# Kernel optimization log

Measured on AMD Instinct MI355X. Metric: run time of the kernel, lower is better.

The kernel has to match this reference:

```python
import jax, jax.numpy as jnp
import numpy as np

SIGMA = 2.5
B, L, V, C = 8, 2048, 8192, 64
F = 2 * (C + 1)  # top_net in_features = 130


def rbf_interp(points_1, feats_1, points_2, sigma):
    """RBF interpolation of feats_1 at points_1 onto points_2 (atom2D torch_rbf, concat=True).
    points_1: [V,3], feats_1: [V,C], points_2: [L,3] -> [L, C+1]
    """
    # exact cdist via gram trick, [L, V]
    d2 = (jnp.sum(points_2 * points_2, -1)[:, None]
          - 2.0 * (points_2 @ points_1.T)
          + jnp.sum(points_1 * points_1, -1)[None, :])
    d = jnp.sqrt(jnp.maximum(d2, 0.0))
    w = jnp.exp(-d / sigma)                       # [L, V]
    dens = jnp.sum(w, axis=1, keepdims=True)      # [L, 1]
    w = w / dens
    # original computes weights under torch.no_grad()
    w = jax.lax.stop_gradient(w)
    dens = jax.lax.stop_gradient(dens)
    feats_2 = w @ feats_1                         # [L, C]
    return jnp.concatenate([feats_2, dens], axis=1)


def setup_inputs() -> dict:
    key = jax.random.key(0)
    ks = jax.random.split(key, 8)
    return {
        "locs_left": jax.random.normal(ks[0], (B, L, 3), jnp.float32),
        "locs_right": jax.random.normal(ks[1], (B, L, 3), jnp.float32),
        "verts_left": jax.random.normal(ks[2], (B, V, 3), jnp.float32),
        "verts_right": jax.random.normal(ks[3], (B, V, 3), jnp.float32),
        "feats_left": jax.random.normal(ks[4], (B, V, C), jnp.float32),
        "feats_right": jax.random.normal(ks[5], (B, V, C), jnp.float32),
        "w1": jax.random.normal(ks[6], (F, F), jnp.float32) * (1.0 / np.sqrt(F)),
        "b1": jnp.zeros((F,), jnp.float32),
        "w2": jax.random.normal(ks[7], (1, F), jnp.float32) * (1.0 / np.sqrt(F)),
        "b2": jnp.zeros((1,), jnp.float32),
    }


def reference(locs_left, locs_right, verts_left, verts_right,
              feats_left, feats_right, w1, b1, w2, b2):
    interp = jax.vmap(lambda p1, f1, p2: rbf_interp(p1, f1, p2, SIGMA))
    fl = interp(verts_left, feats_left, locs_left)     # [B, L, C+1]
    fr = interp(verts_right, feats_right, locs_right)  # [B, L, C+1]
    x = jnp.concatenate([fl, fr], axis=-1)             # [B, L, 2*(C+1)]
    h = jax.nn.relu(x @ w1.T + b1)                     # dropout inactive at eval
    out = h @ w2.T + b2                                # [B, L, 1]
    return out.reshape(-1)                             # [B*L]
```

## Files before the change

kernel.cpp:

```cpp
#include <hip/hip_runtime.h>
#include <hip/hip_bf16.h>
#include <stdint.h>

#define B_ 8
#define L_ 2048
#define V_ 8192
#define C_ 64
#define F_ 130

typedef float    f32x4  __attribute__((ext_vector_type(4)));
typedef float    f32x2  __attribute__((ext_vector_type(2)));
typedef short    s16x8  __attribute__((ext_vector_type(8)));
typedef __bf16   bf16x8 __attribute__((ext_vector_type(8)));
typedef uint32_t u32x4  __attribute__((ext_vector_type(4)));

#if __has_builtin(__builtin_amdgcn_exp2f)
#define EXP2(x) __builtin_amdgcn_exp2f(x)
#else
#define EXP2(x) exp2f(x)
#endif

#if __has_builtin(__builtin_elementwise_fma)
#define PK_FMA4(a,b,c) __builtin_elementwise_fma((a),(b),(c))
#else
__device__ __forceinline__ f32x4 PK_FMA4(f32x4 a, f32x4 b, f32x4 c) {
  f32x4 r; for (int i=0;i<4;++i) r[i]=fmaf(a[i],b[i],c[i]); return r;
}
#endif
#if __has_builtin(__builtin_elementwise_max)
#define PK_MAX4(a,b) __builtin_elementwise_max((a),(b))
#else
__device__ __forceinline__ f32x4 PK_MAX4(f32x4 a, f32x4 b) {
  f32x4 r; for (int i=0;i<4;++i) r[i]=fmaxf(a[i],b[i]); return r;
}
#endif

constexpr float KEXP2 = (float)(0.57707801635558535 * 0.57707801635558535);

__device__ __forceinline__ uint32_t pack2bf(float a, float b) {
  uint16_t ua = __builtin_bit_cast(uint16_t, (__bf16)a);
  uint16_t ub = __builtin_bit_cast(uint16_t, (__bf16)b);
  return (uint32_t)ua | ((uint32_t)ub << 16);
}

__device__ __forceinline__ float wave_sum(float v) {
  v += __shfl_xor(v, 1);  v += __shfl_xor(v, 2);  v += __shfl_xor(v, 4);
  v += __shfl_xor(v, 8);  v += __shfl_xor(v, 16); v += __shfl_xor(v, 32);
  return v;
}

__device__ __forceinline__ void gload_lds16(const void* g, void* l) {
  __builtin_amdgcn_global_load_lds(
      (const __attribute__((address_space(1))) void*)g,
      (__attribute__((address_space(3))) void*)l, 16, 0, 0);
}

__global__ __launch_bounds__(256) void pre_kernel(
    const float* __restrict__ verts_l, const float* __restrict__ verts_r,
    const float* __restrict__ feats_l, const float* __restrict__ feats_r,
    uint16_t* __restrict__ fT2, float* __restrict__ vS2)
{
  __shared__ float fs[64][68];
  const int blk = blockIdx.x, tid = threadIdx.x;
  if (blk < 1024) {
    const int p = blk >> 6, kt2 = blk & 63;
    const int side = p >> 3, bb = p & 7;
    const float* src = (side ? feats_r : feats_l) + (size_t)bb * (V_ * C_);
    #pragma unroll
    for (int sub = 0; sub < 2; ++sub) {
      const int ktile = kt2 * 2 + sub;
      const int v0 = ktile * 64;
      {
        const int sv = tid >> 2, c0 = (tid & 3) * 16;
        const int m = ((sv >> 3) & 7) << 3;
        const float* s = src + (size_t)(v0 + sv) * C_ + c0;
        f32x4 a = *(const f32x4*)(s);
        f32x4 b = *(const f32x4*)(s + 4);
        f32x4 c = *(const f32x4*)(s + 8);
        f32x4 d = *(const f32x4*)(s + 12);
        *(f32x4*)&fs[sv][(c0)      ^ m] = a;
        *(f32x4*)&fs[sv][(c0 + 4)  ^ m] = b;
        *(f32x4*)&fs[sv][(c0 + 8)  ^ m] = c;
        *(f32x4*)&fs[sv][(c0 + 12) ^ m] = d;
      }
      __syncthreads();
      {
        char* tb = (char*)fT2 + ((size_t)p * 128 + ktile) * 8192;
        #pragma unroll
        for (int half = 0; half < 2; ++half) {
          const int r  = half * 256 + tid;
          const int ch = r >> 3;
          const int kq = (r & 7) ^ (ch & 7);
          const int cs = ch ^ (kq << 3);
          const int row0 = kq * 8;
          float f[8];
          #pragma unroll
          for (int e = 0; e < 8; ++e) f[e] = fs[row0 + e][cs];
          u32x4 val = { pack2bf(f[0], f[1]), pack2bf(f[2], f[3]),
                        pack2bf(f[4], f[5]), pack2bf(f[6], f[7]) };
          *(u32x4*)(tb + r * 16) = val;
        }
      }
      __syncthreads();
    }
  } else {
    const int blk2 = blk - 1024;
    const int p = blk2 >> 5, chunk = blk2 & 31;
    const int side = p >> 3, bb = p & 7;
    const float* src = (side ? verts_r : verts_l) + (size_t)bb * (V_ * 3);
    const int v = chunk * 256 + tid;
    const float x = src[v * 3 + 0], y = src[v * 3 + 1], z = src[v * 3 + 2];
    const float n2 = x * x + y * y + z * z;
    constexpr float M2K = -2.0f * KEXP2;
    float* d = vS2 + (size_t)p * 32768 + (size_t)(v >> 6) * 256 + (v & 63);
    d[0] = M2K * x; d[64] = M2K * y; d[128] = M2K * z; d[192] = KEXP2 * n2;
  }
}

__global__ __launch_bounds__(512, 6) void fused_kernel(
    const float* __restrict__ locs_l, const float* __restrict__ locs_r,
    const uint16_t* __restrict__ fT2, const float* __restrict__ vS2,
    const float* __restrict__ w1, const float* __restrict__ b1,
    const float* __restrict__ w2, const float* __restrict__ b2,
    float* __restrict__ outp)
{
  __shared__ __align__(16) char  flds[2][16384];
  __shared__ __align__(16) float vlds[2][2][4][64];
  __shared__ __align__(16) float xs[32][132];
  __shared__ float densp[32];

  const int bid  = blockIdx.x;
  const int bb   = bid & 7;
  const int tile = bid >> 3;
  const int tid  = threadIdx.x;
  const int wid  = tid >> 6, lane = tid & 63;
  const int g    = wid & 1, h = wid >> 1;
  const int ln15 = lane & 15, lg = lane >> 4;
  const int xorv = (ln15 & 7) << 4;
  const f32x4 zero4 = {0.f, 0.f, 0.f, 0.f};

  const int sub  = h >> 1;
  const int hh   = h & 1;
  const int abfix = sub * 8192 + ln15 * 128 + ((((hh << 2) | lg) << 4) ^ xorv);

  for (int s = 0; s < 2; ++s) {
    const int p = s * 8 + bb;
    const float* locs = (s ? locs_r : locs_l) + (size_t)bb * (L_ * 3);
    const int arow = tile * 32 + g * 16 + ln15;
    const float px = locs[arow * 3 + 0];
    const float py = locs[arow * 3 + 1];
    const float pz = locs[arow * 3 + 2];
    const float pn2p = KEXP2 * (px * px + py * py + pz * pz);
    const f32x4 px4 = {px, px, px, px};
    const f32x4 py4 = {py, py, py, py};
    const f32x4 pz4 = {pz, pz, pz, pz};
    const f32x4 pn4 = {pn2p, pn2p, pn2p, pn2p};

    const char* ftp = (const char*)fT2 + (size_t)p * (128 * 8192);
    const char* vtp = (const char*)vS2 + (size_t)p * (128 * 1024);

    f32x4 acc0 = zero4, acc1 = zero4, acc2 = zero4, acc3 = zero4;
    f32x4 densa = zero4;

    gload_lds16(ftp + wid * 2048 + lane * 16,        &flds[0][wid * 2048]);
    gload_lds16(ftp + wid * 2048 + 1024 + lane * 16, &flds[0][wid * 2048 + 1024]);
    if (wid < 2) gload_lds16(vtp + wid * 1024 + lane * 16, &vlds[0][wid][0][0]);
    __syncthreads();

    const char* gfn = ftp + 16384 + wid * 2048 + lane * 16;
    const char* gvn = vtp + 2048  + wid * 1024 + lane * 16;

    for (int kt = 0; kt < 64; ++kt) {
      const int cur = kt & 1;
      if (kt < 63) {
        const int nxt = cur ^ 1;
        gload_lds16(gfn,        &flds[nxt][wid * 2048]);
        gload_lds16(gfn + 1024, &flds[nxt][wid * 2048 + 1024]);
        if (wid < 2) gload_lds16(gvn, &vlds[nxt][wid][0][0]);
        gfn += 16384;
        gvn += 2048;
      }
      const int kof = hh * 32 + lg * 8;
      const f32x4 vxa = *(const f32x4*)&vlds[cur][sub][0][kof];
      const f32x4 vxb = *(const f32x4*)&vlds[cur][sub][0][kof + 4];
      const f32x4 vya = *(const f32x4*)&vlds[cur][sub][1][kof];
      const f32x4 vyb = *(const f32x4*)&vlds[cur][sub][1][kof + 4];
      const f32x4 vza = *(const f32x4*)&vlds[cur][sub][2][kof];
      const f32x4 vzb = *(const f32x4*)&vlds[cur][sub][2][kof + 4];
      const f32x4 vna = *(const f32x4*)&vlds[cur][sub][3][kof];
      const f32x4 vnb = *(const f32x4*)&vlds[cur][sub][3][kof + 4];

      f32x4 d2a = PK_FMA4(vza, pz4, vna + pn4);
      d2a = PK_FMA4(vya, py4, d2a);
      d2a = PK_FMA4(vxa, px4, d2a);
      d2a = PK_MAX4(d2a, zero4);
      f32x4 d2b = PK_FMA4(vzb, pz4, vnb + pn4);
      d2b = PK_FMA4(vyb, py4, d2b);
      d2b = PK_FMA4(vxb, px4, d2b);
      d2b = PK_MAX4(d2b, zero4);

      f32x4 wa, wb;
      #pragma unroll
      for (int e = 0; e < 4; ++e) {
        wa[e] = EXP2(-__builtin_amdgcn_sqrtf(d2a[e]));
        wb[e] = EXP2(-__builtin_amdgcn_sqrtf(d2b[e]));
      }
      densa += wa;
      densa += wb;
      bf16x8 av;
      #pragma unroll
      for (int e = 0; e < 4; ++e) {
        av[e]     = (__bf16)wa[e];
        av[e + 4] = (__bf16)wb[e];
      }
      const s16x8 afrag = __builtin_bit_cast(s16x8, av);
      const char* fl = flds[cur];
      const s16x8 bf0 = *(const s16x8*)(fl + abfix);
      const s16x8 bf1 = *(const s16x8*)(fl + abfix + 2048);
      const s16x8 bf2 = *(const s16x8*)(fl + abfix + 4096);
      const s16x8 bf3 = *(const s16x8*)(fl + abfix + 6144);
      acc0 = __builtin_amdgcn_mfma_f32_16x16x32_bf16(afrag, bf0, acc0, 0, 0, 0);
      acc1 = __builtin_amdgcn_mfma_f32_16x16x32_bf16(afrag, bf1, acc1, 0, 0, 0);
      acc2 = __builtin_amdgcn_mfma_f32_16x16x32_bf16(afrag, bf2, acc2, 0, 0, 0);
      acc3 = __builtin_amdgcn_mfma_f32_16x16x32_bf16(afrag, bf3, acc3, 0, 0, 0);
      __syncthreads();
    }

    float dens = (densa.x + densa.y) + (densa.z + densa.w);
    dens += __shfl_xor(dens, 16);
    dens += __shfl_xor(dens, 32);

    #pragma unroll
    for (int ph = 0; ph < 4; ++ph) {
      if (h == ph) {
        if (ph == 0) {
          if (lane < 16) densp[g * 16 + lane] = dens;
          #pragma unroll
          for (int r = 0; r < 4; ++r) {
            const int row = g * 16 + lg * 4 + r;
            xs[row][s * 65 +      ln15] = acc0[r];
            xs[row][s * 65 + 16 + ln15] = acc1[r];
            xs[row][s * 65 + 32 + ln15] = acc2[r];
            xs[row][s * 65 + 48 + ln15] = acc3[r];
          }
        } else {
          if (lane < 16) densp[g * 16 + lane] += dens;
          #pragma unroll
          for (int r = 0; r < 4; ++r) {
            const int row = g * 16 + lg * 4 + r;
            xs[row][s * 65 +      ln15] += acc0[r];
            xs[row][s * 65 + 16 + ln15] += acc1[r];
            xs[row][s * 65 + 32 + ln15] += acc2[r];
            xs[row][s * 65 + 48 + ln15] += acc3[r];
          }
        }
      }
      __syncthreads();
    }
    for (int idx = tid; idx < 32 * 64; idx += 512) {
      const int row = idx >> 6, c = idx & 63;
      xs[row][s * 65 + c] *= (1.0f / densp[row]);
    }
    if (tid < 32) xs[tid][s * 65 + 64] = densp[tid];
    __syncthreads();
  }

  const int r0 = wid * 4;
  float hh0[4] = {0.f,0.f,0.f,0.f}, hh1[4] = {0.f,0.f,0.f,0.f};
  const float* wr0 = w1 + (size_t)lane * F_;
  const float* wr1 = w1 + (size_t)(lane + 64) * F_;

  #pragma unroll 4
  for (int i = 0; i < 128; i += 4) {
    const f32x2 a01 = *(const f32x2*)&wr0[i];
    const f32x2 a23 = *(const f32x2*)&wr0[i + 2];
    const f32x2 c01 = *(const f32x2*)&wr1[i];
    const f32x2 c23 = *(const f32x2*)&wr1[i + 2];
    #pragma unroll
    for (int r = 0; r < 4; ++r) {
      const f32x4 xv = *(const f32x4*)&xs[r0 + r][i];
      hh0[r] = fmaf(xv.x, a01.x, hh0[r]); hh0[r] = fmaf(xv.y, a01.y, hh0[r]);
      hh0[r] = fmaf(xv.z, a23.x, hh0[r]); hh0[r] = fmaf(xv.w, a23.y, hh0[r]);
      hh1[r] = fmaf(xv.x, c01.x, hh1[r]); hh1[r] = fmaf(xv.y, c01.y, hh1[r]);
      hh1[r] = fmaf(xv.z, c23.x, hh1[r]); hh1[r] = fmaf(xv.w, c23.y, hh1[r]);
    }
  }
  {
    const float a0 = wr0[128], a1 = wr0[129];
    const float c0 = wr1[128], c1 = wr1[129];
    #pragma unroll
    for (int r = 0; r < 4; ++r) {
      const float x0 = xs[r0 + r][128], x1 = xs[r0 + r][129];
      hh0[r] = fmaf(x0, a0, fmaf(x1, a1, hh0[r]));
      hh1[r] = fmaf(x0, c0, fmaf(x1, c1, hh1[r]));
    }
  }
  const float* wr2 = w1 + 128 * F_;
  const float* wr3 = w1 + 129 * F_;
  float hp2[4], hp3[4];
  #pragma unroll
  for (int r = 0; r < 4; ++r) {
    const float xa = xs[r0 + r][lane];
    const float xb = xs[r0 + r][lane + 64];
    float p2 = wr2[lane] * xa + wr2[lane + 64] * xb;
    float p3 = wr3[lane] * xa + wr3[lane + 64] * xb;
    if (lane < 2) {
      const float xc = xs[r0 + r][128 + lane];
      p2 += wr2[128 + lane] * xc;
      p3 += wr3[128 + lane] * xc;
    }
    hp2[r] = wave_sum(p2);
    hp3[r] = wave_sum(p3);
  }
  const float b1a = b1[lane], b1b = b1[lane + 64];
  const float w2a = w2[lane], w2b = w2[lane + 64];
  const float b1c = b1[128], b1d = b1[129];
  const float w2c = w2[128], w2d = w2[129];
  const float b2v = b2[0];
  #pragma unroll
  for (int r = 0; r < 4; ++r) {
    float o = w2a * fmaxf(hh0[r] + b1a, 0.f) + w2b * fmaxf(hh1[r] + b1b, 0.f);
    o = wave_sum(o);
    if (lane == 0) {
      o += w2c * fmaxf(hp2[r] + b1c, 0.f) + w2d * fmaxf(hp3[r] + b1d, 0.f);
      outp[(size_t)bb * L_ + tile * 32 + r0 + r] = o + b2v;
    }
  }
}

extern "C" void kernel_launch(void* const* d_in, const int* in_sizes, int n_in,
                              void* d_out, int out_size, void* d_ws, size_t ws_size,
                              hipStream_t stream) {
  const float* locs_l  = (const float*)d_in[0];
  const float* locs_r  = (const float*)d_in[1];
  const float* verts_l = (const float*)d_in[2];
  const float* verts_r = (const float*)d_in[3];
  const float* feats_l = (const float*)d_in[4];
  const float* feats_r = (const float*)d_in[5];
  const float* w1 = (const float*)d_in[6];
  const float* b1 = (const float*)d_in[7];
  const float* w2 = (const float*)d_in[8];
  const float* b2 = (const float*)d_in[9];

  char* ws = (char*)d_ws;
  uint16_t* fT2 = (uint16_t*)ws;
  float*    vS2 = (float*)(ws + 16777216);
  float*    out = (float*)d_out;

  pre_kernel<<<1536, 256, 0, stream>>>(verts_l, verts_r, feats_l, feats_r, fT2, vS2);
  fused_kernel<<<512, 512, 0, stream>>>(locs_l, locs_r, fT2, vS2,
                                        w1, b1, w2, b2, out);
}
```

Baseline: 226.0 us.

## Load vertex data into registers and use triple-buffered LDS with single barrier

Vertex coordinate tiles are now loaded directly from global memory into registers, double-buffered across unrolled iterations, instead of being staged through LDS. The feature tile pipeline moves to three LDS buffers, with an explicit vmcnt wait and one raw s_barrier per step, replacing the per-iteration __syncthreads. The goal is to cut LDS traffic and synchronization stalls so global loads overlap the exp/MFMA work. In exchange it uses more LDS and registers, and lowers launch bounds from 6 to 4 waves, which may reduce occupancy. The hand-set vmcnt(10) count is fragile and could break correctness if the compiler emits a different number of loads.

```diff
diff --git a/kernel.cpp b/kernel.cpp
--- a/kernel.cpp
+++ b/kernel.cpp
@@ -117,15 +117,18 @@
   }
 }
 
-__global__ __launch_bounds__(512, 6) void fused_kernel(
+struct VRegs {
+  f32x4 xa, xb, ya, yb, za, zb, na, nb;
+};
+
+__global__ __launch_bounds__(512, 4) void fused_kernel(
     const float* __restrict__ locs_l, const float* __restrict__ locs_r,
     const uint16_t* __restrict__ fT2, const float* __restrict__ vS2,
     const float* __restrict__ w1, const float* __restrict__ b1,
     const float* __restrict__ w2, const float* __restrict__ b2,
     float* __restrict__ outp)
 {
-  __shared__ __align__(16) char  flds[2][16384];
-  __shared__ __align__(16) float vlds[2][2][4][64];
+  __shared__ __align__(16) char  flds[3][16384];
   __shared__ __align__(16) float xs[32][132];
   __shared__ float densp[32];
 
@@ -142,6 +145,7 @@
   const int sub  = h >> 1;
   const int hh   = h & 1;
   const int abfix = sub * 8192 + ln15 * 128 + ((((hh << 2) | lg) << 4) ^ xorv);
+  const int voff = hh * 32 + lg * 8;
 
   for (int s = 0; s < 2; ++s) {
     const int p = s * 8 + bb;
@@ -156,49 +160,29 @@
     const f32x4 pz4 = {pz, pz, pz, pz};
     const f32x4 pn4 = {pn2p, pn2p, pn2p, pn2p};
 
-    const char* ftp = (const char*)fT2 + (size_t)p * (128 * 8192);
-    const char* vtp = (const char*)vS2 + (size_t)p * (128 * 1024);
+    const char*  ftp = (const char*)fT2 + (size_t)p * (128 * 8192);
+    const float* vtp = vS2 + (size_t)p * 32768 + sub * 256 + voff;
 
     f32x4 acc0 = zero4, acc1 = zero4, acc2 = zero4, acc3 = zero4;
     f32x4 densa = zero4;
 
-    gload_lds16(ftp + wid * 2048 + lane * 16,        &flds[0][wid * 2048]);
-    gload_lds16(ftp + wid * 2048 + 1024 + lane * 16, &flds[0][wid * 2048 + 1024]);
-    if (wid < 2) gload_lds16(vtp + wid * 1024 + lane * 16, &vlds[0][wid][0][0]);
-    __syncthreads();
-
-    const char* gfn = ftp + 16384 + wid * 2048 + lane * 16;
-    const char* gvn = vtp + 2048  + wid * 1024 + lane * 16;
-
-    for (int kt = 0; kt < 64; ++kt) {
-      const int cur = kt & 1;
-      if (kt < 63) {
-        const int nxt = cur ^ 1;
-        gload_lds16(gfn,        &flds[nxt][wid * 2048]);
-        gload_lds16(gfn + 1024, &flds[nxt][wid * 2048 + 1024]);
-        if (wid < 2) gload_lds16(gvn, &vlds[nxt][wid][0][0]);
-        gfn += 16384;
-        gvn += 2048;
-      }
-      const int kof = hh * 32 + lg * 8;
-      const f32x4 vxa = *(const f32x4*)&vlds[cur][sub][0][kof];
-      const f32x4 vxb = *(const f32x4*)&vlds[cur][sub][0][kof + 4];
-      const f32x4 vya = *(const f32x4*)&vlds[cur][sub][1][kof];
-      const f32x4 vyb = *(const f32x4*)&vlds[cur][sub][1][kof + 4];
-      const f32x4 vza = *(const f32x4*)&vlds[cur][sub][2][kof];
-      const f32x4 vzb = *(const f32x4*)&vlds[cur][sub][2][kof + 4];
-      const f32x4 vna = *(const f32x4*)&vlds[cur][sub][3][kof];
-      const f32x4 vnb = *(const f32x4*)&vlds[cur][sub][3][kof + 4];
-
-      f32x4 d2a = PK_FMA4(vza, pz4, vna + pn4);
-      d2a = PK_FMA4(vya, py4, d2a);
-      d2a = PK_FMA4(vxa, px4, d2a);
+    auto vload = [&](int k, VRegs& v) {
+      const float* b = vtp + k * 512;
+      v.xa = *(const f32x4*)(b);       v.xb = *(const f32x4*)(b + 4);
+      v.ya = *(const f32x4*)(b + 64);  v.yb = *(const f32x4*)(b + 68);
+      v.za = *(const f32x4*)(b + 128); v.zb = *(const f32x4*)(b + 132);
+      v.na = *(const f32x4*)(b + 192); v.nb = *(const f32x4*)(b + 196);
+    };
+
+    auto body = [&](const VRegs& v, const char* fl) {
+      f32x4 d2a = PK_FMA4(v.za, pz4, v.na + pn4);
+      d2a = PK_FMA4(v.ya, py4, d2a);
+      d2a = PK_FMA4(v.xa, px4, d2a);
       d2a = PK_MAX4(d2a, zero4);
-      f32x4 d2b = PK_FMA4(vzb, pz4, vnb + pn4);
-      d2b = PK_FMA4(vyb, py4, d2b);
-      d2b = PK_FMA4(vxb, px4, d2b);
+      f32x4 d2b = PK_FMA4(v.zb, pz4, v.nb + pn4);
+      d2b = PK_FMA4(v.yb, py4, d2b);
+      d2b = PK_FMA4(v.xb, px4, d2b);
       d2b = PK_MAX4(d2b, zero4);
-
       f32x4 wa, wb;
       #pragma unroll
       for (int e = 0; e < 4; ++e) {
@@ -214,7 +198,6 @@
         av[e + 4] = (__bf16)wb[e];
       }
       const s16x8 afrag = __builtin_bit_cast(s16x8, av);
-      const char* fl = flds[cur];
       const s16x8 bf0 = *(const s16x8*)(fl + abfix);
       const s16x8 bf1 = *(const s16x8*)(fl + abfix + 2048);
       const s16x8 bf2 = *(const s16x8*)(fl + abfix + 4096);
@@ -223,8 +206,38 @@
       acc1 = __builtin_amdgcn_mfma_f32_16x16x32_bf16(afrag, bf1, acc1, 0, 0, 0);
       acc2 = __builtin_amdgcn_mfma_f32_16x16x32_bf16(afrag, bf2, acc2, 0, 0, 0);
       acc3 = __builtin_amdgcn_mfma_f32_16x16x32_bf16(afrag, bf3, acc3, 0, 0, 0);
-      __syncthreads();
-    }
+    };
+
+    VRegs vA, vB;
+    vload(0, vA);
+    gload_lds16(ftp + wid * 2048 + lane * 16,        &flds[0][wid * 2048]);
+    gload_lds16(ftp + wid * 2048 + 1024 + lane * 16, &flds[0][wid * 2048 + 1024]);
+
+    const char* gfn = ftp + 16384 + wid * 2048 + lane * 16;
+    int cur = 0, nxt = 1;
+
+    #define STEP(K, VUSE, VLD)                                          \
+      {                                                                 \
+        if ((K) < 63) {                                                 \
+          vload((K) + 1, VLD);                                          \
+          gload_lds16(gfn,        &flds[nxt][wid * 2048]);              \
+          gload_lds16(gfn + 1024, &flds[nxt][wid * 2048 + 1024]);       \
+          gfn += 16384;                                                 \
+          asm volatile("s_waitcnt vmcnt(10)" ::: "memory");             \
+        } else {                                                        \
+          asm volatile("s_waitcnt vmcnt(0)" ::: "memory");              \
+        }                                                               \
+        __builtin_amdgcn_s_barrier();                                   \
+        body(VUSE, flds[cur]);                                          \
+        cur = (cur == 2) ? 0 : cur + 1;                                 \
+        nxt = (nxt == 2) ? 0 : nxt + 1;                                 \
+      }
+
+    for (int kt = 0; kt < 64; kt += 2) {
+      STEP(kt,     vA, vB);
+      STEP(kt + 1, vB, vA);
+    }
+    #undef STEP
 
     float dens = (densa.x + densa.y) + (densa.z + densa.w);
     dens += __shfl_xor(dens, 16);
```

After: 289.5 us. 28.1% more time.
